# Kernel tuning notes

Measured on AMD Instinct MI355X. Metric: run time of the kernel, lower is better.

The kernel has to match this reference:

```python
import jax, jax.numpy as jnp
import numpy as np

B, T, C, NH = 8, 1024, 1024, 16
HD = C // NH
EPS = 1e-5


def setup_inputs() -> dict:
    key = jax.random.key(0)
    k1, k2, k3 = jax.random.split(key, 3)
    x = jax.random.normal(k1, (B, T, C), dtype=jnp.float32)
    past_kv = jax.random.normal(k2, (NH, HD, HD), dtype=jnp.float32) * 0.1
    W_qkv = jax.random.normal(k3, (C, 3 * C), dtype=jnp.float32) * 0.02
    gn_weight = jnp.ones((NH,), dtype=jnp.float32)
    gn_bias = jnp.zeros((NH,), dtype=jnp.float32)
    return {"x": x, "past_kv": past_kv, "W_qkv": W_qkv,
            "gn_weight": gn_weight, "gn_bias": gn_bias}


def _decay_mask(nh, t, dtype):
    # decay_mask[h, i, j] = gamma[h]**(i-j) if i >= j else 0
    gamma = 1.0 - 2.0 ** (-5.0 - jnp.arange(nh, dtype=jnp.float32))
    idx = jnp.arange(t)
    diff = idx[:, None] - idx[None, :]            # [T, T]
    mask = diff >= 0
    pow_ = gamma[:, None, None] ** jnp.where(mask, diff, 0).astype(jnp.float32)
    return jnp.where(mask[None], pow_, 0.0).astype(dtype), gamma.astype(dtype)


def reference(x, past_kv, W_qkv, gn_weight, gn_bias):
    b, t, c = x.shape
    nh = gn_weight.shape[0]
    hd = c // nh

    qkv = x @ W_qkv                               # [B, T, 3C]
    q, k, v = jnp.split(qkv, 3, axis=2)
    split_heads = lambda u: u.reshape(b, t, nh, hd).transpose(0, 2, 1, 3)  # [B,nh,T,hd]
    q, k, v = split_heads(q), split_heads(k), split_heads(v)

    decay, gamma = _decay_mask(nh, t, x.dtype)    # [nh,T,T], [nh]

    # intra-chunk: decay-masked QK^T @ V
    ret = jnp.einsum('bhtd,bhsd->bhts', q, k) * decay      # [B,nh,T,T]
    inner = jnp.einsum('bhts,bhsd->bhtd', ret, v)          # [B,nh,T,hd]

    # cross-chunk: q @ past_kv * (n_head * chunk_size)
    inner_decay = float(nh * hd)
    cross = jnp.einsum('bhtd,hde->bhte', q, past_kv) * inner_decay
    r = inner + cross                                      # [B,nh,T,hd]

    # recurrent state update: gamma * past_kv + k^T @ v, then mean over batch
    current_kv = gamma[:, None, None] * past_kv + jnp.einsum('bhtd,bhte->bhde', k, v)
    current_kv = current_kv.mean(axis=0)                   # [nh,hd,hd]

    # GroupNorm(1, n_head) on [B, nh, hd, T] (single group => stats over all non-batch dims)
    y = r.transpose(0, 1, 3, 2)                            # [B,nh,hd,T]
    mu = y.mean(axis=(1, 2, 3), keepdims=True)
    var = y.var(axis=(1, 2, 3), keepdims=True)             # biased, matches torch GroupNorm
    yn = (y - mu) * jax.lax.rsqrt(var + EPS)
    yn = yn * gn_weight[None, :, None, None] + gn_bias[None, :, None, None]

    # rearrange 'b c h t -> b t (c h)'
    out = yn.transpose(0, 3, 1, 2).reshape(b, t, c)
    return out, current_kv
```

## Files before the change

kernel.cpp:

```cpp
#include <hip/hip_runtime.h>


#define TKN 8192
#define N3  3072

typedef short short8 __attribute__((ext_vector_type(8)));
typedef float f32x4 __attribute__((ext_vector_type(4)));

static __device__ __forceinline__ unsigned short f2bf(float f){
  unsigned int u = __float_as_uint(f);
  u += 0x7FFFu + ((u >> 16) & 1u);
  return (unsigned short)(u >> 16);
}
static __device__ __forceinline__ float bf2f(unsigned short s){
  return __uint_as_float(((unsigned int)s) << 16);
}
static __device__ __forceinline__ void g2lds16(const void* g, void* l){
  __builtin_amdgcn_global_load_lds(
      (const __attribute__((address_space(1))) unsigned int*)g,
      (__attribute__((address_space(3))) unsigned int*)l, 16, 0, 0);
}

__global__ __launch_bounds__(256) void k_cvt(const float* __restrict__ x,
                                             const float* __restrict__ w,
                                             const float* __restrict__ pk,
                                             unsigned short* __restrict__ xb,
                                             unsigned short* __restrict__ wt,
                                             unsigned short* __restrict__ pkt){
  __shared__ float tile[64][65];
  const int bid = blockIdx.x;
  if (bid < 2048){
    const int n4 = TKN*1024/4;
    for (int idx = bid*256 + threadIdx.x; idx < n4; idx += 2048*256){
      float4 v = reinterpret_cast<const float4*>(x)[idx];
      ushort4 o;
      o.x = f2bf(v.x); o.y = f2bf(v.y); o.z = f2bf(v.z); o.w = f2bf(v.w);
      reinterpret_cast<ushort4*>(xb)[idx] = o;
    }
  } else if (bid < 2816){
    const int b2 = bid - 2048;
    const int n0 = (b2 % 48)*64, k0 = (b2 / 48)*64;
    const int tn = threadIdx.x & 63, t4 = threadIdx.x >> 6;
    for (int kk = t4; kk < 64; kk += 4)
      tile[kk][tn] = w[(k0+kk)*N3 + n0 + tn];
    __syncthreads();
    for (int nn = t4; nn < 64; nn += 4)
      wt[(n0+nn)*1024 + k0 + tn] = f2bf(tile[tn][nn]);
  } else {
    int i = (bid - 2816)*256 + threadIdx.x;
    int h = i >> 12, e = (i >> 6) & 63, d = i & 63;
    pkt[i] = f2bf(pk[(h<<12) + (d<<6) + e] * 1024.0f);
  }
}

__global__ __launch_bounds__(256, 3) void k_gemm(const unsigned short* __restrict__ A,
                                                 const unsigned short* __restrict__ Bt,
                                                 unsigned short* __restrict__ qb,
                                                 unsigned short* __restrict__ kb,
                                                 unsigned short* __restrict__ vtb){
  __shared__ unsigned short sm[24576];
  char* smb = (char*)sm;
  const int tid = threadIdx.x;
  const int lane = tid & 63, wid = tid >> 6;
  const int wm = wid >> 1, wn = wid & 1;
  const int n15 = lane & 15, l4 = lane >> 4;
  const int m0 = blockIdx.y * 128;
  const int n0 = blockIdx.x * 128;

  f32x4 acc[4][4] = {};

  const int sr0 = tid >> 2,        sq0 = (tid & 3) ^ (sr0 & 3);
  const int sr1 = (tid + 256) >> 2, sq1 = (tid & 3) ^ (sr1 & 3);
  #define STAGE(kt, b) do {                                                            \
    g2lds16(A  + (long)(m0 + sr0)*1024 + (kt)*32 + sq0*8, smb + (b)*8192 + tid*16);    \
    g2lds16(A  + (long)(m0 + sr1)*1024 + (kt)*32 + sq1*8, smb + (b)*8192 + 4096 + tid*16); \
    g2lds16(Bt + (long)(n0 + sr0)*1024 + (kt)*32 + sq0*8, smb + 24576 + (b)*8192 + tid*16); \
    g2lds16(Bt + (long)(n0 + sr1)*1024 + (kt)*32 + sq1*8, smb + 24576 + (b)*8192 + 4096 + tid*16); \
  } while(0)

  STAGE(0, 0);
  STAGE(1, 1);
  asm volatile("s_waitcnt vmcnt(4)" ::: "memory");
  __builtin_amdgcn_s_barrier();

  int cur = 0;
  for (int t = 0; t < 32; ++t){
    int nb = cur + 2; if (nb >= 3) nb -= 3;
    if (t < 30) STAGE(t + 2, nb);
    const char* ab = smb + cur*8192;
    const char* bb = smb + 24576 + cur*8192;
    short8 a[4], b[4];
    #pragma unroll
    for (int i = 0; i < 4; ++i){
      int ra = wm*64 + i*16 + n15;
      a[i] = *(const short8*)(ab + ra*64 + ((l4 ^ (ra & 3)) << 4));
      int rb = wn*64 + i*16 + n15;
      b[i] = *(const short8*)(bb + rb*64 + ((l4 ^ (rb & 3)) << 4));
    }
    __builtin_amdgcn_s_setprio(1);
    #pragma unroll
    for (int i = 0; i < 4; ++i)
      #pragma unroll
      for (int j = 0; j < 4; ++j)
        acc[i][j] = __builtin_amdgcn_mfma_f32_16x16x32_bf16(a[i], b[j], acc[i][j], 0, 0, 0);
    __builtin_amdgcn_s_setprio(0);
    if (t < 30) asm volatile("s_waitcnt vmcnt(4)" ::: "memory");
    else        asm volatile("s_waitcnt vmcnt(0)" ::: "memory");
    __builtin_amdgcn_s_barrier();
    cur = cur + 1; if (cur == 3) cur = 0;
  }
  #undef STAGE

  const int bb2 = m0 >> 10;
  const int which = n0 >> 10;
  const int cw = (n0 & 1023) + wn*64;
  const int h = cw >> 6;
  const long bh = (long)(bb2*16 + h);
  const int trow0 = (m0 & 1023) + wm*64;
  char* W = smb + wid*8192;

  if (which < 2){
    unsigned short* dst = which ? kb : qb;
    #pragma unroll
    for (int mi = 0; mi < 4; ++mi)
      #pragma unroll
      for (int nf = 0; nf < 4; ++nf)
        #pragma unroll
        for (int r = 0; r < 4; ++r){
          int row = mi*16 + l4*4 + r;
          int colb = (nf*32 + 2*n15) ^ ((row & 7) << 4);
          *(unsigned short*)(W + row*128 + colb) = f2bf(acc[mi][nf][r]);
        }
    asm volatile("s_waitcnt lgkmcnt(0)" ::: "memory");
    #pragma unroll
    for (int hh = 0; hh < 2; ++hh)
      #pragma unroll
      for (int c2 = 0; c2 < 4; ++c2){
        int row = hh*32 + (lane >> 1);
        int off = ((lane & 1)*64 + c2*16) ^ ((row & 7) << 4);
        uint4 v = *(const uint4*)(W + row*128 + off);
        int dcol = (lane & 1)*32 + c2*8;
        *(uint4*)(&dst[(bh*1024 + trow0 + row)*64 + dcol]) = v;
      }
  } else {
    #pragma unroll
    for (int mi = 0; mi < 4; ++mi)
      #pragma unroll
      for (int nf = 0; nf < 4; ++nf)
        #pragma unroll
        for (int r = 0; r < 4; ++r){
          int dl = nf*16 + n15;
          int row = mi*16 + l4*4 + r;
          int colb = (2*row) ^ ((dl & 7) << 4);
          *(unsigned short*)(W + dl*128 + colb) = f2bf(acc[mi][nf][r]);
        }
    asm volatile("s_waitcnt lgkmcnt(0)" ::: "memory");
    #pragma unroll
    for (int hh = 0; hh < 2; ++hh)
      #pragma unroll
      for (int c2 = 0; c2 < 4; ++c2){
        int dl = hh*32 + (lane >> 1);
        int off = ((lane & 1)*64 + c2*16) ^ ((dl & 7) << 4);
        uint4 v = *(const uint4*)(W + dl*128 + off);
        int tcol = (lane & 1)*32 + c2*8;
        *(uint4*)(&vtb[(bh*64 + dl)*1024 + trow0 + tcol]) = v;
      }
  }
}

__global__ __launch_bounds__(256) void k_attn(const unsigned short* __restrict__ qb,
                                              const unsigned short* __restrict__ kb,
                                              const unsigned short* __restrict__ vtb,
                                              const unsigned short* __restrict__ pkt,
                                              unsigned short* __restrict__ rb,
                                              float* __restrict__ gnp){
  __shared__ unsigned short Qs[8192];
  __shared__ unsigned short Kd[2][4096];
  __shared__ unsigned short Vd[2][4096];
  __shared__ unsigned short Ps[8192];
  __shared__ float gred[2][4];
  const int qpair = blockIdx.x;
  const int bh = blockIdx.y;
  const int h = bh & 15;
  const int tid = threadIdx.x;
  const int lane = tid & 63, wid = tid >> 6;
  const int n15 = lane & 15, l4 = lane >> 4;
  const unsigned short* qp = qb + (long)bh*65536;
  const unsigned short* kp = kb + (long)bh*65536;
  const unsigned short* vp = vtb + (long)bh*65536;
  const float lg = log2f(1.0f - exp2f(-5.0f - (float)h));
  const int srow = tid >> 3, schunk = tid & 7;

  float cexp[4];
  #pragma unroll
  for (int nf = 0; nf < 4; ++nf)
    cexp[nf] = exp2f(-lg * (float)(nf*16 + n15));

  float gs = 0.f, gq = 0.f;
  unsigned short* rp = rb + (long)bh*65536;

  for (int p = 0; p < 2; ++p){
    const int qt = p ? (7 - qpair) : qpair;
    const int t0 = qt * 128;
    for (int c = 0; c < 4; ++c){
      int r = c*32 + srow;
      int src = schunk ^ (r & 7);
      g2lds16(qp + (long)(t0 + r)*64 + src*8, (char*)Qs + c*4096 + tid*16);
    }
    for (int c = 0; c < 2; ++c){
      int r = c*32 + srow;
      int src = schunk ^ (r & 7);
      g2lds16(pkt + (long)(h*64 + r)*64 + src*8, (char*)Ps + c*4096 + tid*16);
      g2lds16(kp + (long)r*64 + src*8, (char*)Kd[0] + c*4096 + tid*16);
      g2lds16(vp + (long)r*1024 + src*8, (char*)Vd[0] + c*4096 + tid*16);
    }
    asm volatile("s_waitcnt vmcnt(0)" ::: "memory");
    __syncthreads();

    short8 aq[2][2];
    #pragma unroll
    for (int mf = 0; mf < 2; ++mf)
      #pragma unroll
      for (int kk = 0; kk < 2; ++kk){
        int r = wid*32 + mf*16 + n15;
        int sl = (kk*4 + l4) ^ (r & 7);
        aq[mf][kk] = *reinterpret_cast<const short8*>((const char*)Qs + r*128 + sl*16);
      }

    f32x4 o[2][4] = {};
    #pragma unroll
    for (int kk = 0; kk < 2; ++kk){
      short8 bpk[4];
      #pragma unroll
      for (int nf = 0; nf < 4; ++nf){
        int r = nf*16 + n15;
        int sl = (kk*4 + l4) ^ (r & 7);
        bpk[nf] = *reinterpret_cast<const short8*>((const char*)Ps + r*128 + sl*16);
      }
      #pragma unroll
      for (int mf = 0; mf < 2; ++mf)
        #pragma unroll
        for (int nf = 0; nf < 4; ++nf)
          o[mf][nf] = __builtin_amdgcn_mfma_f32_16x16x32_bf16(aq[mf][kk], bpk[nf], o[mf][nf], 0,0,0);
    }
    __syncthreads();

    const int jmax = 2*qt + 1;
    int cur = 0;
    for (int j = 0; j <= jmax; ++j){
      const int kv0 = j*64;
      if (j < jmax){
        const int kvn = kv0 + 64;
        for (int c = 0; c < 2; ++c){
          int r = c*32 + srow;
          int src = schunk ^ (r & 7);
          g2lds16(kp + (long)(kvn + r)*64 + src*8, (char*)Kd[cur^1] + c*4096 + tid*16);
          g2lds16(vp + (long)r*1024 + kvn + src*8, (char*)Vd[cur^1] + c*4096 + tid*16);
        }
      }
      f32x4 s[2][4] = {};
      #pragma unroll
      for (int kk = 0; kk < 2; ++kk){
        short8 bk[4];
        #pragma unroll
        for (int nf = 0; nf < 4; ++nf){
          int r = nf*16 + n15;
          int sl = (kk*4 + l4) ^ (r & 7);
          bk[nf] = *reinterpret_cast<const short8*>((const char*)Kd[cur] + r*128 + sl*16);
        }
        #pragma unroll
        for (int mf = 0; mf < 2; ++mf)
          #pragma unroll
          for (int nf = 0; nf < 4; ++nf)
            s[mf][nf] = __builtin_amdgcn_mfma_f32_16x16x32_bf16(aq[mf][kk], bk[nf], s[mf][nf], 0,0,0);
      }
      float rowf[2][4];
      #pragma unroll
      for (int mf = 0; mf < 2; ++mf){
        int mB = wid*32 + mf*16 + l4*4;
        #pragma unroll
        for (int r = 0; r < 4; ++r)
          rowf[mf][r] = exp2f(lg * (float)(t0 + mB + r - kv0));
      }
      if (kv0 >= t0){
        #pragma unroll
        for (int mf = 0; mf < 2; ++mf){
          int mB = wid*32 + mf*16 + l4*4;
          #pragma unroll
          for (int nf = 0; nf < 4; ++nf){
            int tj = kv0 + nf*16 + n15;
            int n = nf*16 + n15;
            #pragma unroll
            for (int r = 0; r < 4; ++r){
              int ti = t0 + mB + r;
              float val = (ti >= tj) ? s[mf][nf][r] * (rowf[mf][r] * cexp[nf]) : 0.0f;
              int byte = ((mB + r)*128 + n*2) ^ (((mB + r) & 7) << 4);
              *(unsigned short*)((char*)Ps + byte) = f2bf(val);
            }
          }
        }
      } else {
        #pragma unroll
        for (int mf = 0; mf < 2; ++mf){
          int mB = wid*32 + mf*16 + l4*4;
          #pragma unroll
          for (int nf = 0; nf < 4; ++nf){
            int n = nf*16 + n15;
            #pragma unroll
            for (int r = 0; r < 4; ++r){
              float val = s[mf][nf][r] * (rowf[mf][r] * cexp[nf]);
              int byte = ((mB + r)*128 + n*2) ^ (((mB + r) & 7) << 4);
              *(unsigned short*)((char*)Ps + byte) = f2bf(val);
            }
          }
        }
      }
      #pragma unroll
      for (int kk = 0; kk < 2; ++kk){
        short8 ap[2], bv[4];
        #pragma unroll
        for (int mf = 0; mf < 2; ++mf){
          int r = wid*32 + mf*16 + n15;
          int sl = (kk*4 + l4) ^ (r & 7);
          ap[mf] = *reinterpret_cast<const short8*>((const char*)Ps + r*128 + sl*16);
        }
        #pragma unroll
        for (int nf = 0; nf < 4; ++nf){
          int r = nf*16 + n15;
          int sl = (kk*4 + l4) ^ (r & 7);
          bv[nf] = *reinterpret_cast<const short8*>((const char*)Vd[cur] + r*128 + sl*16);
        }
        #pragma unroll
        for (int mf = 0; mf < 2; ++mf)
          #pragma unroll
          for (int nf = 0; nf < 4; ++nf)
            o[mf][nf] = __builtin_amdgcn_mfma_f32_16x16x32_bf16(ap[mf], bv[nf], o[mf][nf], 0,0,0);
      }
      asm volatile("s_waitcnt vmcnt(0)" ::: "memory");
      __syncthreads();
      cur ^= 1;
    }
    #pragma unroll
    for (int mf = 0; mf < 2; ++mf)
      #pragma unroll
      for (int nf = 0; nf < 4; ++nf)
        #pragma unroll
        for (int r = 0; r < 4; ++r){
          int t = t0 + wid*32 + mf*16 + l4*4 + r;
          int d = nf*16 + n15;
          float v = o[mf][nf][r];
          rp[t*64 + d] = f2bf(v);
          gs += v; gq += v*v;
        }
  }
  #pragma unroll
  for (int off = 32; off > 0; off >>= 1){
    gs += __shfl_down(gs, off);
    gq += __shfl_down(gq, off);
  }
  if (lane == 0){ gred[0][wid] = gs; gred[1][wid] = gq; }
  __syncthreads();
  if (tid == 0){
    gnp[(bh*4 + qpair)*2]   = gred[0][0]+gred[0][1]+gred[0][2]+gred[0][3];
    gnp[(bh*4 + qpair)*2+1] = gred[1][0]+gred[1][1]+gred[1][2]+gred[1][3];
  }
}

__global__ __launch_bounds__(256) void k_kvpart(const unsigned short* __restrict__ kb,
                                                const unsigned short* __restrict__ vtb,
                                                float* __restrict__ part){
  __shared__ unsigned short Kt[64*64];
  __shared__ unsigned int   Vt32[64*33];
  const int tc = blockIdx.x, bh = blockIdx.y;
  const int tid = threadIdx.x;
  const int d0 = (tid >> 4) << 2;
  const int e0 = (tid & 15) << 2;
  const unsigned short* kp = kb + (long)bh*65536;
  const unsigned short* vp = vtb + (long)bh*65536;
  float acc[4][4] = {{0.f}};
  for (int tt = 0; tt < 4; ++tt){
    const int tb = tc*256 + tt*64;
    __syncthreads();
    {
      int rr0 = tid >> 3, off = (tid & 7) * 8;
      for (int c = 0; c < 2; ++c){
        int r = c*32 + rr0;
        *reinterpret_cast<uint4*>(&Kt[r*64 + off]) =
            *reinterpret_cast<const uint4*>(&kp[(long)(tb + r)*64 + off]);
        uint4 vv = *reinterpret_cast<const uint4*>(&vp[(long)r*1024 + tb + off]);
        unsigned int* dv = &Vt32[r*33 + (off >> 1)];
        dv[0] = vv.x; dv[1] = vv.y; dv[2] = vv.z; dv[3] = vv.w;
      }
    }
    __syncthreads();
    const unsigned short* Vt = (const unsigned short*)Vt32;
    for (int t = 0; t < 64; ++t){
      float kv[4], vv[4];
      #pragma unroll
      for (int i = 0; i < 4; ++i) kv[i] = bf2f(Kt[t*64 + d0 + i]);
      #pragma unroll
      for (int i = 0; i < 4; ++i) vv[i] = bf2f(Vt[(e0 + i)*66 + t]);
      #pragma unroll
      for (int i = 0; i < 4; ++i)
        #pragma unroll
        for (int j = 0; j < 4; ++j) acc[i][j] += kv[i]*vv[j];
    }
  }
  float* pp = part + ((long)(tc*128 + bh) << 12);
  for (int i = 0; i < 4; ++i)
    for (int j = 0; j < 4; ++j)
      pp[(d0+i)*64 + e0 + j] = acc[i][j];
}

__global__ __launch_bounds__(256) void k_kvfin(const float* __restrict__ part,
                                               const float* __restrict__ pk,
                                               float* __restrict__ okv,
                                               const float* __restrict__ gnp,
                                               float* __restrict__ musig){
  if (blockIdx.x == 0 && threadIdx.x < 8){
    int b = threadIdx.x;
    float S = 0.f, Q = 0.f;
    for (int g = 0; g < 64; ++g){ S += gnp[b*128 + g*2]; Q += gnp[b*128 + g*2 + 1]; }
    float mu  = S * (1.0f/1048576.0f);
    float var = Q * (1.0f/1048576.0f) - mu*mu;
    musig[b*2]   = mu;
    musig[b*2+1] = rsqrtf(var + 1e-5f);
  }
  int i = blockIdx.x*256 + threadIdx.x;
  int h = i >> 12;
  float acc = 0.f;
  for (int tc = 0; tc < 4; ++tc)
    for (int b = 0; b < 8; ++b)
      acc += part[((long)(tc*128 + b*16 + h) << 12) + (i & 4095)];
  float gamma = 1.0f - exp2f(-5.0f - (float)h);
  okv[i] = gamma * pk[i] + acc * 0.125f;
}

__global__ __launch_bounds__(256) void k_gnnorm(const unsigned short* __restrict__ rbuf,
                                                const float* __restrict__ musig,
                                                const float* __restrict__ gw,
                                                const float* __restrict__ gb,
                                                float* __restrict__ out){
  const int n8 = TKN*1024/8;
  for (int idx = blockIdx.x*256 + threadIdx.x; idx < n8; idx += gridDim.x*256){
    int o = idx*8;
    int c = o & 1023;
    int t = (o >> 10) & 1023;
    int b = o >> 20;
    int h = c >> 6, d = c & 63;
    short8 v = *reinterpret_cast<const short8*>(rbuf + ((long)(b*16 + h) << 16) + t*64 + d);
    float rs = musig[b*2+1];
    float a = gw[h]*rs, b2 = gb[h] - musig[b*2]*a;
    float4 o0, o1;
    o0.x = bf2f((unsigned short)v[0])*a + b2;
    o0.y = bf2f((unsigned short)v[1])*a + b2;
    o0.z = bf2f((unsigned short)v[2])*a + b2;
    o0.w = bf2f((unsigned short)v[3])*a + b2;
    o1.x = bf2f((unsigned short)v[4])*a + b2;
    o1.y = bf2f((unsigned short)v[5])*a + b2;
    o1.z = bf2f((unsigned short)v[6])*a + b2;
    o1.w = bf2f((unsigned short)v[7])*a + b2;
    *reinterpret_cast<float4*>(out + o)     = o0;
    *reinterpret_cast<float4*>(out + o + 4) = o1;
  }
}

extern "C" void kernel_launch(void* const* d_in, const int* in_sizes, int n_in,
                              void* d_out, int out_size, void* d_ws, size_t ws_size,
                              hipStream_t stream){
  const float* x  = (const float*)d_in[0];
  const float* pk = (const float*)d_in[1];
  const float* w  = (const float*)d_in[2];
  const float* gw = (const float*)d_in[3];
  const float* gb = (const float*)d_in[4];
  float* out = (float*)d_out;
  char* ws = (char*)d_ws;

  unsigned short* Xb  = (unsigned short*)(ws);
  unsigned short* WTb = (unsigned short*)(ws + 16777216);
  unsigned short* Qb  = (unsigned short*)(ws + 23068672);
  unsigned short* Kb  = (unsigned short*)(ws + 39845888);
  unsigned short* VTb = (unsigned short*)(ws + 56623104);
  unsigned short* PKt = (unsigned short*)(ws + 73400320);
  unsigned short* Rb  = (unsigned short*)(ws + 73531392);
  float* KVp = (float*)(ws);
  float* GNp = (float*)(ws + 90308608);
  float* MuS = (float*)(ws + 90312704);

  k_cvt    <<<dim3(3072),    dim3(256), 0, stream>>>(x, w, pk, Xb, WTb, PKt);
  k_gemm   <<<dim3(24, 64),  dim3(256), 0, stream>>>(Xb, WTb, Qb, Kb, VTb);
  k_attn   <<<dim3(4, 128),  dim3(256), 0, stream>>>(Qb, Kb, VTb, PKt, Rb, GNp);
  k_kvpart <<<dim3(4, 128),  dim3(256), 0, stream>>>(Kb, VTb, KVp);
  k_kvfin  <<<dim3(256),     dim3(256), 0, stream>>>(KVp, pk, out + 8388608, GNp, MuS);
  k_gnnorm <<<dim3(1024),    dim3(256), 0, stream>>>(Rb, MuS, gw, gb, out);
}
```

Measured before the change: 183.6 us.

## Rework GEMM LDS swizzle, transpose QK tiles, skip masked waves, stage output stores

The QKV GEMM gets a new row permutation and XOR swizzle for the LDS staging and fragment reads, meant to cut LDS bank conflicts. The retention kernel now computes S transposed so each lane holds four consecutive key columns. That allows packed 8-byte bf16 writes of the decayed scores and per-lane decay factors. Waves whose query rows lie entirely above the current KV tile skip the QK and PV work, and the masking branch runs only on diagonal tiles. Output rows are staged through LDS so global writes become coalesced 16-byte stores, at the cost of an extra barrier per query tile.

New measurement: 163.6 us. -10.9%, faster.

```diff
diff --git a/kernel.cpp b/kernel.cpp
--- a/kernel.cpp
+++ b/kernel.cpp
@@ -69,13 +69,14 @@
 
   f32x4 acc[4][4] = {};
 
-  const int sr0 = tid >> 2,        sq0 = (tid & 3) ^ (sr0 & 3);
-  const int sr1 = (tid + 256) >> 2, sq1 = (tid & 3) ^ (sr1 & 3);
-  #define STAGE(kt, b) do {                                                            \
-    g2lds16(A  + (long)(m0 + sr0)*1024 + (kt)*32 + sq0*8, smb + (b)*8192 + tid*16);    \
-    g2lds16(A  + (long)(m0 + sr1)*1024 + (kt)*32 + sq1*8, smb + (b)*8192 + 4096 + tid*16); \
-    g2lds16(Bt + (long)(n0 + sr0)*1024 + (kt)*32 + sq0*8, smb + 24576 + (b)*8192 + tid*16); \
-    g2lds16(Bt + (long)(n0 + sr1)*1024 + (kt)*32 + sq1*8, smb + 24576 + (b)*8192 + 4096 + tid*16); \
+  const int l0 = tid >> 2;
+  const int r0 = (l0 & ~3) | ((l0 & 1) << 1) | ((l0 >> 1) & 1);
+  const int c0 = (((tid & 3) ^ ((tid >> 4) & 3)) << 3);
+  #define STAGE(kt, b) do {                                                              \
+    g2lds16(A  + (long)(m0 + r0)*1024      + (kt)*32 + c0, smb + (b)*8192 + tid*16);     \
+    g2lds16(A  + (long)(m0 + 64 + r0)*1024 + (kt)*32 + c0, smb + (b)*8192 + 4096 + tid*16); \
+    g2lds16(Bt + (long)(n0 + r0)*1024      + (kt)*32 + c0, smb + 24576 + (b)*8192 + tid*16); \
+    g2lds16(Bt + (long)(n0 + 64 + r0)*1024 + (kt)*32 + c0, smb + 24576 + (b)*8192 + 4096 + tid*16); \
   } while(0)
 
   STAGE(0, 0);
@@ -83,6 +84,7 @@
   asm volatile("s_waitcnt vmcnt(4)" ::: "memory");
   __builtin_amdgcn_s_barrier();
 
+  const int slb = (l4 ^ ((n15 >> 2) & 3)) << 4;
   int cur = 0;
   for (int t = 0; t < 32; ++t){
     int nb = cur + 2; if (nb >= 3) nb -= 3;
@@ -93,9 +95,11 @@
     #pragma unroll
     for (int i = 0; i < 4; ++i){
       int ra = wm*64 + i*16 + n15;
-      a[i] = *(const short8*)(ab + ra*64 + ((l4 ^ (ra & 3)) << 4));
+      int rs = (ra & ~3) | ((ra & 1) << 1) | ((ra >> 1) & 1);
+      a[i] = *(const short8*)(ab + rs*64 + slb);
       int rb = wn*64 + i*16 + n15;
-      b[i] = *(const short8*)(bb + rb*64 + ((l4 ^ (rb & 3)) << 4));
+      int rbs = (rb & ~3) | ((rb & 1) << 1) | ((rb >> 1) & 1);
+      b[i] = *(const short8*)(bb + rbs*64 + slb);
     }
     __builtin_amdgcn_s_setprio(1);
     #pragma unroll
@@ -191,10 +195,12 @@
   const float lg = log2f(1.0f - exp2f(-5.0f - (float)h));
   const int srow = tid >> 3, schunk = tid & 7;
 
-  float cexp[4];
+  float kvE[4][4];
   #pragma unroll
-  for (int nf = 0; nf < 4; ++nf)
-    cexp[nf] = exp2f(-lg * (float)(nf*16 + n15));
+  for (int i = 0; i < 4; ++i)
+    #pragma unroll
+    for (int r = 0; r < 4; ++r)
+      kvE[i][r] = exp2f(-lg * (float)(i*16 + l4*4 + r));
 
   float gs = 0.f, gq = 0.f;
   unsigned short* rp = rb + (long)bh*65536;
@@ -258,83 +264,71 @@
           g2lds16(vp + (long)r*1024 + kvn + src*8, (char*)Vd[cur^1] + c*4096 + tid*16);
         }
       }
-      f32x4 s[2][4] = {};
-      #pragma unroll
-      for (int kk = 0; kk < 2; ++kk){
-        short8 bk[4];
-        #pragma unroll
-        for (int nf = 0; nf < 4; ++nf){
-          int r = nf*16 + n15;
-          int sl = (kk*4 + l4) ^ (r & 7);
-          bk[nf] = *reinterpret_cast<const short8*>((const char*)Kd[cur] + r*128 + sl*16);
-        }
-        #pragma unroll
-        for (int mf = 0; mf < 2; ++mf)
-          #pragma unroll
-          for (int nf = 0; nf < 4; ++nf)
-            s[mf][nf] = __builtin_amdgcn_mfma_f32_16x16x32_bf16(aq[mf][kk], bk[nf], s[mf][nf], 0,0,0);
-      }
-      float rowf[2][4];
-      #pragma unroll
-      for (int mf = 0; mf < 2; ++mf){
-        int mB = wid*32 + mf*16 + l4*4;
-        #pragma unroll
-        for (int r = 0; r < 4; ++r)
-          rowf[mf][r] = exp2f(lg * (float)(t0 + mB + r - kv0));
-      }
-      if (kv0 >= t0){
+      const bool active = (kv0 <= t0 + wid*32 + 31);
+      if (active){
+        f32x4 sT[4][2] = {};
+        #pragma unroll
+        for (int kk = 0; kk < 2; ++kk){
+          short8 bk[4];
+          #pragma unroll
+          for (int i = 0; i < 4; ++i){
+            int r = i*16 + n15;
+            int sl = (kk*4 + l4) ^ (r & 7);
+            bk[i] = *reinterpret_cast<const short8*>((const char*)Kd[cur] + r*128 + sl*16);
+          }
+          #pragma unroll
+          for (int i = 0; i < 4; ++i)
+            #pragma unroll
+            for (int mf = 0; mf < 2; ++mf)
+              sT[i][mf] = __builtin_amdgcn_mfma_f32_16x16x32_bf16(bk[i], aq[mf][kk], sT[i][mf], 0,0,0);
+        }
+        const bool diag = (kv0 + 63 > t0 + wid*32);
         #pragma unroll
         for (int mf = 0; mf < 2; ++mf){
-          int mB = wid*32 + mf*16 + l4*4;
+          const int trow = wid*32 + mf*16 + n15;
+          const float rowE = exp2f(lg * (float)(t0 + trow - kv0));
+          char* wb = (char*)Ps + trow*128;
+          const int swz = (trow & 7) << 4;
+          #pragma unroll
+          for (int i = 0; i < 4; ++i){
+            float v0 = sT[i][mf][0] * (rowE * kvE[i][0]);
+            float v1 = sT[i][mf][1] * (rowE * kvE[i][1]);
+            float v2 = sT[i][mf][2] * (rowE * kvE[i][2]);
+            float v3 = sT[i][mf][3] * (rowE * kvE[i][3]);
+            if (diag){
+              int dd = (t0 + trow) - (kv0 + i*16 + l4*4);
+              if (dd < 0) v0 = 0.f;
+              if (dd < 1) v1 = 0.f;
+              if (dd < 2) v2 = 0.f;
+              if (dd < 3) v3 = 0.f;
+            }
+            uint2 pw;
+            pw.x = (unsigned int)f2bf(v0) | ((unsigned int)f2bf(v1) << 16);
+            pw.y = (unsigned int)f2bf(v2) | ((unsigned int)f2bf(v3) << 16);
+            *(uint2*)(wb + ((i*32 + l4*8) ^ swz)) = pw;
+          }
+        }
+        #pragma unroll
+        for (int kk = 0; kk < 2; ++kk){
+          short8 ap[2], bv[4];
+          #pragma unroll
+          for (int mf = 0; mf < 2; ++mf){
+            int r = wid*32 + mf*16 + n15;
+            int sl = (kk*4 + l4) ^ (r & 7);
+            ap[mf] = *reinterpret_cast<const short8*>((const char*)Ps + r*128 + sl*16);
+          }
           #pragma unroll
           for (int nf = 0; nf < 4; ++nf){
-            int tj = kv0 + nf*16 + n15;
-            int n = nf*16 + n15;
+            int r = nf*16 + n15;
+            int sl = (kk*4 + l4) ^ (r & 7);
+            bv[nf] = *reinterpret_cast<const short8*>((const char*)Vd[cur] + r*128 + sl*16);
+          }
+          #pragma unroll
+          for (int mf = 0; mf < 2; ++mf)
             #pragma unroll
-            for (int r = 0; r < 4; ++r){
-              int ti = t0 + mB + r;
-              float val = (ti >= tj) ? s[mf][nf][r] * (rowf[mf][r] * cexp[nf]) : 0.0f;
-              int byte = ((mB + r)*128 + n*2) ^ (((mB + r) & 7) << 4);
-              *(unsigned short*)((char*)Ps + byte) = f2bf(val);
-            }
-          }
-        }
-      } else {
-        #pragma unroll
-        for (int mf = 0; mf < 2; ++mf){
-          int mB = wid*32 + mf*16 + l4*4;
-          #pragma unroll
-          for (int nf = 0; nf < 4; ++nf){
-            int n = nf*16 + n15;
-            #pragma unroll
-            for (int r = 0; r < 4; ++r){
-              float val = s[mf][nf][r] * (rowf[mf][r] * cexp[nf]);
-              int byte = ((mB + r)*128 + n*2) ^ (((mB + r) & 7) << 4);
-              *(unsigned short*)((char*)Ps + byte) = f2bf(val);
-            }
-          }
-        }
-      }
-      #pragma unroll
-      for (int kk = 0; kk < 2; ++kk){
-        short8 ap[2], bv[4];
-        #pragma unroll
-        for (int mf = 0; mf < 2; ++mf){
-          int r = wid*32 + mf*16 + n15;
-          int sl = (kk*4 + l4) ^ (r & 7);
-          ap[mf] = *reinterpret_cast<const short8*>((const char*)Ps + r*128 + sl*16);
-        }
-        #pragma unroll
-        for (int nf = 0; nf < 4; ++nf){
-          int r = nf*16 + n15;
-          int sl = (kk*4 + l4) ^ (r & 7);
-          bv[nf] = *reinterpret_cast<const short8*>((const char*)Vd[cur] + r*128 + sl*16);
-        }
-        #pragma unroll
-        for (int mf = 0; mf < 2; ++mf)
-          #pragma unroll
-          for (int nf = 0; nf < 4; ++nf)
-            o[mf][nf] = __builtin_amdgcn_mfma_f32_16x16x32_bf16(ap[mf], bv[nf], o[mf][nf], 0,0,0);
+            for (int nf = 0; nf < 4; ++nf)
+              o[mf][nf] = __builtin_amdgcn_mfma_f32_16x16x32_bf16(ap[mf], bv[nf], o[mf][nf], 0,0,0);
+        }
       }
       asm volatile("s_waitcnt vmcnt(0)" ::: "memory");
       __syncthreads();
@@ -346,12 +340,21 @@
       for (int nf = 0; nf < 4; ++nf)
         #pragma unroll
         for (int r = 0; r < 4; ++r){
-          int t = t0 + wid*32 + mf*16 + l4*4 + r;
+          int trow = wid*32 + mf*16 + l4*4 + r;
           int d = nf*16 + n15;
           float v = o[mf][nf][r];
-          rp[t*64 + d] = f2bf(v);
           gs += v; gq += v*v;
-        }
+          *(unsigned short*)((char*)Ps + trow*128 + ((2*d) ^ ((trow & 7) << 4))) = f2bf(v);
+        }
+    asm volatile("s_waitcnt lgkmcnt(0)" ::: "memory");
+    #pragma unroll
+    for (int rr = 0; rr < 4; ++rr){
+      int row = wid*32 + rr*8 + (lane >> 3);
+      int off = (((lane & 7) << 4) ^ ((row & 7) << 4));
+      uint4 v = *(const uint4*)((const char*)Ps + row*128 + off);
+      *(uint4*)(rp + (long)(t0 + row)*64 + ((lane & 7) << 3)) = v;
+    }
+    __syncthreads();
   }
   #pragma unroll
   for (int off = 32; off > 0; off >>= 1){
```
